# Kernel tuning notes

Measured on AMD Instinct MI355X. Metric: run time of the kernel, lower is better.

Reference implementation:

```python
import jax, jax.numpy as jnp
import numpy as np

NUM_HEADS = 16

def setup_inputs() -> dict:
    key = jax.random.key(0)
    ks = jax.random.split(key, 6)
    B, S, D = 2, 2048, 1024
    scale = 1.0 / np.sqrt(D)
    x = jax.random.normal(ks[0], (B, S, D), dtype=jnp.float32)
    mask = jnp.tril(jnp.ones((S, S), dtype=jnp.int32))[None, None, :, :]  # causal [1,1,S,S]
    Wq = jax.random.normal(ks[1], (D, D), dtype=jnp.float32) * scale
    Wk = jax.random.normal(ks[2], (D, D), dtype=jnp.float32) * scale
    Wv = jax.random.normal(ks[3], (D, D), dtype=jnp.float32) * scale
    Wo = jax.random.normal(ks[4], (D, D), dtype=jnp.float32) * scale
    z = jnp.zeros((D,), dtype=jnp.float32)
    return {"x": x, "mask": mask, "Wq": Wq, "bq": z, "Wk": Wk, "bk": z,
            "Wv": Wv, "bv": z, "Wo": Wo, "bo": z}

def reference(x, mask, Wq, bq, Wk, bk, Wv, bv, Wo, bo):
    B, S, D = x.shape
    H = NUM_HEADS
    hd = D // H
    # torch Linear: y = x @ W.T + b
    def proj(W, b):
        return (x @ W.T + b).reshape(B, S, H, hd).transpose(0, 2, 1, 3)  # [B,H,S,hd]
    q = proj(Wq, bq)
    k = proj(Wk, bk)
    v = proj(Wv, bv)
    # NOTE: original module does NOT scale by 1/sqrt(d_k) -- faithful to source.
    scores = jnp.einsum('bhqd,bhkd->bhqk', q, k)  # [B,H,S,S]
    scores = jnp.where(mask == 0, jnp.float32(-10000.0), scores)
    attn = jax.nn.softmax(scores, axis=-1)
    # dropout omitted for deterministic reference (eval-mode equivalent)
    out = jnp.einsum('bhqk,bhkd->bhqd', attn, v)
    out = out.transpose(0, 2, 1, 3).reshape(B, S, D)
    return out @ Wo.T + bo
```

## Files before the change

### kernel.cpp

```cpp
#include <hip/hip_runtime.h>

#define S_LEN 2048
#define DM    1024
#define NHEAD 16
#define HDIM  64
#define NB    2
#define NROWS (NB * S_LEN)
#define RCP_LN2 1.44269504f

using f32x4  = __attribute__((ext_vector_type(4))) float;
using f16x8  = __attribute__((ext_vector_type(8))) _Float16;

__device__ __forceinline__ ushort f2h(float f) {
  return __builtin_bit_cast(ushort, (_Float16)f);
}
__device__ __forceinline__ unsigned pkrtz(float a, float b) {
  return __builtin_bit_cast(unsigned, __builtin_amdgcn_cvt_pkrtz(a, b));
}
__device__ __forceinline__ float fexp2(float x) {
  return __builtin_amdgcn_exp2f(x);
}
__device__ __forceinline__ f32x4 mfma16(f16x8 a, f16x8 b, f32x4 c) {
  return __builtin_amdgcn_mfma_f32_16x16x32_f16(a, b, c, 0, 0, 0);
}
__device__ __forceinline__ void async16(const ushort* g, ushort* l) {
  __builtin_amdgcn_global_load_lds(
      (const __attribute__((address_space(1))) unsigned*)g,
      (__attribute__((address_space(3))) unsigned*)l, 16, 0, 0);
}

__device__ const int g_qi_tab[24] = {15,15,7,14,14,13,13,6,12,12,11,11,
                                     5,10,10,9,9,4,8,8,3,2,1,0};
__device__ const int g_hf_tab[24] = {0,1,2,0,1,0,1,2,0,1,0,1,
                                     2,0,1,0,1,2,0,1,2,2,2,2};

__global__ void tohalf5(const float* __restrict__ x,  const float* __restrict__ wq,
                        const float* __restrict__ wk, const float* __restrict__ wv,
                        const float* __restrict__ wo,
                        ushort* __restrict__ Xh, ushort* __restrict__ Wh,
                        ushort* __restrict__ Woh) {
  constexpr int X4 = (NROWS * DM) / 4;
  constexpr int W4 = (DM * DM) / 4;
  const size_t WN = (size_t)DM * DM;
  int i = blockIdx.x * 256 + threadIdx.x;
  const float4* src; ushort4* dst; int k;
  if (i < X4)               { src = (const float4*)x;  dst = (ushort4*)Xh;        k = i; }
  else if (i < X4 + W4)     { src = (const float4*)wq; dst = (ushort4*)Wh;        k = i - X4; }
  else if (i < X4 + 2*W4)   { src = (const float4*)wk; dst = (ushort4*)(Wh+WN);   k = i - X4 - W4; }
  else if (i < X4 + 3*W4)   { src = (const float4*)wv; dst = (ushort4*)(Wh+2*WN); k = i - X4 - 2*W4; }
  else                      { src = (const float4*)wo; dst = (ushort4*)Woh;       k = i - X4 - 3*W4; }
  float4 v = src[k];
  dst[k] = make_ushort4(f2h(v.x), f2h(v.y), f2h(v.z), f2h(v.w));
}

template<int EPI, int MFRAG, int NFRAG>
__global__ __launch_bounds__(256, 2)
void gemm_half(const ushort* __restrict__ A, const ushort* __restrict__ B,
               const float* __restrict__ biasQ, const float* __restrict__ biasK,
               const float* __restrict__ biasV,
               float* __restrict__ outF,
               ushort* __restrict__ Q, ushort* __restrict__ Kd,
               ushort* __restrict__ Vt, int Ncols)
{
  constexpr int KD = 1024;
  constexpr int BM = MFRAG * 32, BN = NFRAG * 32;
  constexpr int NCH = (BM + BN) / 8;
  constexpr int CPW = NCH / 4;
  __shared__ ushort sL[(BM + BN) * 64];
  const int t = threadIdx.x;
  const int w = t >> 6, l = t & 63;
  const int lr = l >> 4, lc = l & 15;
  const int wr = w >> 1, wc = w & 1;
  const int nwg = gridDim.x * gridDim.y;
  const int lin = blockIdx.y * gridDim.x + blockIdx.x;
  const int per8 = nwg >> 3;
  const int swz = (lin & 7) * per8 + (lin >> 3);
  const int i0 = (swz / gridDim.x) * BM, j0 = (swz % gridDim.x) * BN;

  const int srow = l >> 3;
  const int se   = ((l & 7) ^ srow) << 3;

  const ushort* sp[CPW];
#pragma unroll
  for (int ii = 0; ii < CPW; ++ii) {
    const int c = w * CPW + ii;
    sp[ii] = (c < BM / 8)
        ? A + (size_t)(i0 + c * 8 + srow) * KD + se
        : B + (size_t)(j0 + (c - BM / 8) * 8 + srow) * KD + se;
  }

  f32x4 acc[MFRAG][NFRAG] = {};

  for (int k0 = 0; k0 < KD; k0 += 64) {
#pragma unroll
    for (int ii = 0; ii < CPW; ++ii) {
      async16(sp[ii], &sL[(w * CPW + ii) * 512]);
      sp[ii] += 64;
    }
    asm volatile("s_waitcnt vmcnt(0)" ::: "memory");
    __syncthreads();
#pragma unroll
    for (int kk = 0; kk < 2; ++kk) {
      const int cb = (kk * 64 + lr * 16) ^ ((lc & 7) << 4);
      f16x8 a[MFRAG], b[NFRAG];
#pragma unroll
      for (int m = 0; m < MFRAG; ++m)
        a[m] = *(const f16x8*)&sL[(wr * MFRAG * 16 + m * 16 + lc) * 64 + (cb >> 1)];
#pragma unroll
      for (int n = 0; n < NFRAG; ++n)
        b[n] = *(const f16x8*)&sL[BM * 64 + (wc * NFRAG * 16 + n * 16 + lc) * 64 + (cb >> 1)];
      __builtin_amdgcn_s_setprio(1);
#pragma unroll
      for (int m = 0; m < MFRAG; ++m)
#pragma unroll
        for (int n = 0; n < NFRAG; ++n)
          acc[m][n] = mfma16(a[m], b[n], acc[m][n]);
      __builtin_amdgcn_s_setprio(0);
    }
    __syncthreads();
  }

#pragma unroll
  for (int m = 0; m < MFRAG; ++m)
#pragma unroll
    for (int n = 0; n < NFRAG; ++n) {
      const int jbase = j0 + wc * NFRAG * 16 + n * 16;
      const int ibase = i0 + wr * MFRAG * 16 + m * 16 + lr * 4;
      if constexpr (EPI == 0) {
        const int region = jbase >> 10;
        const int jc0 = jbase & 1023;
        const int h = jc0 >> 6, d0 = jc0 & 63;
        const int b = ibase >> 11, s0 = ibase & 2047;
        const size_t bh = (size_t)(b * NHEAD + h);
        if (region == 0) {
          float bb = biasQ[jc0 + lc];
#pragma unroll
          for (int r = 0; r < 4; ++r)
            Q[(bh * S_LEN + s0 + r) * HDIM + d0 + lc] =
                f2h((acc[m][n][r] + bb) * RCP_LN2);
        } else if (region == 1) {
          float bb = biasK[jc0 + lc];
#pragma unroll
          for (int r = 0; r < 4; ++r)
            Kd[(bh * S_LEN + s0 + r) * HDIM + d0 + lc] = f2h(acc[m][n][r] + bb);
        } else {
          float bb = biasV[jc0 + lc];
          ushort4 pv = make_ushort4(f2h(acc[m][n][0] + bb), f2h(acc[m][n][1] + bb),
                                    f2h(acc[m][n][2] + bb), f2h(acc[m][n][3] + bb));
          *(ushort4*)&Vt[(bh * HDIM + d0 + lc) * S_LEN + s0] = pv;
        }
      } else {
#pragma unroll
        for (int r = 0; r < 4; ++r)
          outF[(size_t)(ibase + r) * Ncols + jbase + lc] =
              acc[m][n][r] + biasQ[jbase + lc];
      }
    }
}

__global__ __launch_bounds__(256, 3)
void attn_kernel(const ushort* __restrict__ Qp, const ushort* __restrict__ Kp,
                 const ushort* __restrict__ Vt, ushort* __restrict__ O,
                 float* __restrict__ Pacc, float* __restrict__ Pml)
{
  __shared__ ushort sKV[2][2 * 64 * 64];
  __shared__ ushort Plds[4][2][16][72];
  const int blk = blockIdx.x;
  const int c = blk & 255, s3 = blk >> 8;
  const int rank = (s3 == 0) ? c : ((s3 == 1) ? 511 - c : 512 + c);
  const int ty = rank >> 5, bh = rank & 31;
  const int qi = g_qi_tab[ty], hf = g_hf_tab[ty];
  const int nkt = 2 * qi + 2;
  const int kt0 = (hf == 1) ? (nkt >> 1) : 0;
  const int kt1 = (hf == 0) ? (nkt >> 1) : nkt;

  const int t = threadIdx.x, w = t >> 6, l = t & 63;
  const int g = l >> 4, q = l & 15;
  const size_t base = (size_t)bh * S_LEN * HDIM;
  const int q0w = qi * 128 + w * 32;

  const int srow = l >> 3;
  const int se   = ((l & 7) ^ srow) << 3;

  const int sel = w >> 1;
  const ushort* sp[4];
  const int sadv = (sel == 0) ? 64 * HDIM : 64;
#pragma unroll
  for (int ii = 0; ii < 4; ++ii) {
    const int sub = (w * 4 + ii) & 7;
    sp[ii] = (sel == 0)
        ? Kp + base + (size_t)(kt0 * 64 + sub * 8 + srow) * HDIM + se
        : Vt + ((size_t)bh * HDIM + sub * 8 + srow) * S_LEN + kt0 * 64 + se;
  }

  auto stage = [&](int buf) {
#pragma unroll
    for (int ii = 0; ii < 4; ++ii) {
      const int sub = (w * 4 + ii) & 7;
      async16(sp[ii], &sKV[buf][sel * 4096 + sub * 512]);
      sp[ii] += sadv;
    }
  };

  f16x8 bQ[2][2];
#pragma unroll
  for (int u = 0; u < 2; ++u)
#pragma unroll
    for (int ks = 0; ks < 2; ++ks)
      bQ[u][ks] = *(const f16x8*)(Qp + base +
                  (size_t)(q0w + u * 16 + q) * HDIM + ks * 32 + g * 8);

  f32x4 oacc[2][4] = {};
  float m[2] = {-3e38f, -3e38f}, lsum[2] = {0.f, 0.f};

  stage(0);
  asm volatile("s_waitcnt vmcnt(0)" ::: "memory");
  __syncthreads();
  int cur = 0;

  for (int kt = kt0; kt < kt1; ++kt) {
    if (kt + 1 < kt1) stage(cur ^ 1);

    if (kt * 64 <= q0w + 31) {
      f32x4 s[2][4] = {};
      __builtin_amdgcn_s_setprio(1);
#pragma unroll
      for (int ks = 0; ks < 2; ++ks) {
        const int cb = (((ks * 64 + g * 16) ^ ((q & 7) << 4)) >> 1);
#pragma unroll
        for (int n = 0; n < 4; ++n) {
          f16x8 kf = *(const f16x8*)&sKV[cur][(n * 16 + q) * 64 + cb];
          s[0][n] = mfma16(kf, bQ[0][ks], s[0][n]);
          s[1][n] = mfma16(kf, bQ[1][ks], s[1][n]);
        }
      }
      __builtin_amdgcn_s_setprio(0);
#pragma unroll
      for (int u = 0; u < 2; ++u) {
        if (kt * 64 + 63 > q0w + u * 16) {
          const int qg = q0w + u * 16 + q;
#pragma unroll
          for (int n = 0; n < 4; ++n)
#pragma unroll
            for (int r = 0; r < 4; ++r) {
              int kg = kt * 64 + n * 16 + g * 4 + r;
              if (kg > qg) s[u][n][r] = -1e30f;
            }
        }
      }
      float pm[2];
#pragma unroll
      for (int u = 0; u < 2; ++u) {
        float p = -3e38f;
#pragma unroll
        for (int n = 0; n < 4; ++n)
          p = fmaxf(p, fmaxf(fmaxf(s[u][n][0], s[u][n][1]),
                             fmaxf(s[u][n][2], s[u][n][3])));
        pm[u] = p;
      }
#pragma unroll
      for (int u = 0; u < 2; ++u) {
        if (__any(pm[u] > m[u] + 8.0f)) {
          float pf = pm[u];
          pf = fmaxf(pf, __shfl_xor(pf, 16));
          pf = fmaxf(pf, __shfl_xor(pf, 32));
          float mnew = fmaxf(m[u], pf);
          float sc = fexp2(m[u] - mnew);
          m[u] = mnew;
          float scr[4];
#pragma unroll
          for (int r = 0; r < 4; ++r) scr[r] = __shfl(sc, g * 4 + r);
#pragma unroll
          for (int dt = 0; dt < 4; ++dt)
#pragma unroll
            for (int r = 0; r < 4; ++r) oacc[u][dt][r] *= scr[r];
          lsum[u] *= sc;
        }
      }
#pragma unroll
      for (int u = 0; u < 2; ++u) {
        float rs = 0.f;
#pragma unroll
        for (int n = 0; n < 4; ++n)
#pragma unroll
          for (int r = 0; r < 4; ++r) {
            float pe = fexp2(s[u][n][r] - m[u]);
            s[u][n][r] = pe;
            rs += pe;
          }
        lsum[u] += rs;
      }
#pragma unroll
      for (int u = 0; u < 2; ++u)
#pragma unroll
        for (int n = 0; n < 4; ++n) {
          uint2 pk = make_uint2(pkrtz(s[u][n][0], s[u][n][1]),
                                pkrtz(s[u][n][2], s[u][n][3]));
          *(uint2*)&Plds[w][u][q][n * 16 + g * 4] = pk;
        }
      __builtin_amdgcn_s_setprio(1);
#pragma unroll
      for (int ks = 0; ks < 2; ++ks) {
        const int cb = (((ks * 64 + g * 16) ^ ((q & 7) << 4)) >> 1);
        f16x8 ap0 = *(const f16x8*)&Plds[w][0][q][ks * 32 + g * 8];
        f16x8 ap1 = *(const f16x8*)&Plds[w][1][q][ks * 32 + g * 8];
#pragma unroll
        for (int dt = 0; dt < 4; ++dt) {
          f16x8 bv = *(const f16x8*)&sKV[cur][4096 + (dt * 16 + q) * 64 + cb];
          oacc[0][dt] = mfma16(ap0, bv, oacc[0][dt]);
          oacc[1][dt] = mfma16(ap1, bv, oacc[1][dt]);
        }
      }
      __builtin_amdgcn_s_setprio(0);
    }
    asm volatile("s_waitcnt vmcnt(0)" ::: "memory");
    __syncthreads();
    cur ^= 1;
  }

#pragma unroll
  for (int u = 0; u < 2; ++u) {
    lsum[u] += __shfl_xor(lsum[u], 16);
    lsum[u] += __shfl_xor(lsum[u], 32);
  }

  if (hf == 2) {
    const int b = bh >> 4, h = bh & 15;
#pragma unroll
    for (int u = 0; u < 2; ++u) {
      float lsr[4];
#pragma unroll
      for (int r = 0; r < 4; ++r)
        lsr[r] = __builtin_amdgcn_rcpf(__shfl(lsum[u], g * 4 + r));
#pragma unroll
      for (int dt = 0; dt < 4; ++dt)
#pragma unroll
        for (int r = 0; r < 4; ++r) {
          int qg = q0w + u * 16 + g * 4 + r;
          O[((size_t)b * S_LEN + qg) * DM + h * HDIM + dt * 16 + q] =
              f2h(oacc[u][dt][r] * lsr[r]);
        }
    }
  } else {
    const int pidx = (bh * 8 + (qi - 8)) * 2 + hf;
    float* po = Pacc + (size_t)pidx * (128 * 64);
#pragma unroll
    for (int u = 0; u < 2; ++u) {
#pragma unroll
      for (int dt = 0; dt < 4; ++dt)
#pragma unroll
        for (int r = 0; r < 4; ++r)
          po[(w * 32 + u * 16 + g * 4 + r) * 64 + dt * 16 + q] = oacc[u][dt][r];
      if (g == 0) {
        Pml[(size_t)pidx * 256 + (w * 32 + u * 16 + q) * 2]     = m[u];
        Pml[(size_t)pidx * 256 + (w * 32 + u * 16 + q) * 2 + 1] = lsum[u];
      }
    }
  }
}

__global__ void combine_kernel(const float* __restrict__ Pacc,
                               const float* __restrict__ Pml,
                               ushort* __restrict__ O)
{
  int gid = blockIdx.x * 256 + threadIdx.x;
  int row = gid >> 6, col = gid & 63;
  int bh = row >> 10;
  int rr = row & 1023;
  int qi = 8 + (rr >> 7), qr = rr & 127;
  int p0 = (bh * 8 + (qi - 8)) * 2;
  float m1 = Pml[(size_t)p0 * 256 + qr * 2];
  float l1 = Pml[(size_t)p0 * 256 + qr * 2 + 1];
  float m2 = Pml[(size_t)(p0 + 1) * 256 + qr * 2];
  float l2 = Pml[(size_t)(p0 + 1) * 256 + qr * 2 + 1];
  float o1 = Pacc[(size_t)p0 * 8192 + qr * 64 + col];
  float o2 = Pacc[(size_t)(p0 + 1) * 8192 + qr * 64 + col];
  float mf = fmaxf(m1, m2);
  float e1 = fexp2(m1 - mf), e2 = fexp2(m2 - mf);
  float o = o1 * e1 + o2 * e2;
  float lden = l1 * e1 + l2 * e2;
  int b = bh >> 4, h = bh & 15;
  O[((size_t)b * S_LEN + qi * 128 + qr) * DM + h * HDIM + col] = f2h(o / lden);
}

extern "C" void kernel_launch(void* const* d_in, const int* in_sizes, int n_in,
                              void* d_out, int out_size, void* d_ws, size_t ws_size,
                              hipStream_t stream)
{
  const float* x  = (const float*)d_in[0];
  const float* Wq = (const float*)d_in[2];
  const float* bq = (const float*)d_in[3];
  const float* Wk = (const float*)d_in[4];
  const float* bk = (const float*)d_in[5];
  const float* Wv = (const float*)d_in[6];
  const float* bv = (const float*)d_in[7];
  const float* Wo = (const float*)d_in[8];
  const float* bo = (const float*)d_in[9];
  float* out = (float*)d_out;

  char* ws = (char*)d_ws;
  size_t off = 0;
  auto alloc = [&](size_t bytes) { char* p = ws + off; off += bytes; return p; };
  const size_t XN = (size_t)NROWS * DM;
  const size_t WN = (size_t)DM * DM;

  ushort* Xh  = (ushort*)alloc(XN * 2);
  ushort* Wh  = (ushort*)alloc(3 * WN * 2);
  ushort* Woh = (ushort*)alloc(WN * 2);
  ushort* Qb  = (ushort*)alloc(XN * 2);
  ushort* Kb  = (ushort*)alloc(XN * 2);
  ushort* Vt  = (ushort*)alloc(XN * 2);
  ushort* Ob  = (ushort*)alloc(XN * 2);
  float*  Pacc = (float*)alloc((size_t)512 * 128 * 64 * 4);
  float*  Pml  = (float*)alloc((size_t)512 * 256 * 4);
  (void)ws_size; (void)in_sizes; (void)n_in; (void)out_size;

  const int total4 = (int)(XN / 4 + 4 * (WN / 4));
  tohalf5<<<total4 / 256, 256, 0, stream>>>(x, Wq, Wk, Wv, Wo, Xh, Wh, Woh);

  gemm_half<0, 4, 4><<<dim3(24, 32), 256, 0, stream>>>(
      Xh, Wh, bq, bk, bv, nullptr, Qb, Kb, Vt, 3072);
  attn_kernel<<<768, 256, 0, stream>>>(Qb, Kb, Vt, Ob, Pacc, Pml);
  combine_kernel<<<8192, 256, 0, stream>>>(Pacc, Pml, Ob);
  gemm_half<1, 2, 2><<<dim3(16, 64), 256, 0, stream>>>(
      Ob, Woh, bo, nullptr, nullptr, out, nullptr, nullptr, nullptr, 1024);
}
```

Baseline: 101.8 us.

## Rebalance causal attention into 38 KV-split work units with universal combine

```diff
diff --git a/kernel.cpp b/kernel.cpp
--- a/kernel.cpp
+++ b/kernel.cpp
@@ -7,12 +7,16 @@
 #define NB    2
 #define NROWS (NB * S_LEN)
 #define RCP_LN2 1.44269504f
+#define NTY   38
 
 using f32x4  = __attribute__((ext_vector_type(4))) float;
 using f16x8  = __attribute__((ext_vector_type(8))) _Float16;
 
 __device__ __forceinline__ ushort f2h(float f) {
   return __builtin_bit_cast(ushort, (_Float16)f);
+}
+__device__ __forceinline__ float h2f(ushort u) {
+  return (float)__builtin_bit_cast(_Float16, u);
 }
 __device__ __forceinline__ unsigned pkrtz(float a, float b) {
   return __builtin_bit_cast(unsigned, __builtin_amdgcn_cvt_pkrtz(a, b));
@@ -29,10 +33,21 @@
       (__attribute__((address_space(3))) unsigned*)l, 16, 0, 0);
 }
 
-__device__ const int g_qi_tab[24] = {15,15,7,14,14,13,13,6,12,12,11,11,
-                                     5,10,10,9,9,4,8,8,3,2,1,0};
-__device__ const int g_hf_tab[24] = {0,1,2,0,1,0,1,2,0,1,0,1,
-                                     2,0,1,0,1,2,0,1,2,2,2,2};
+__device__ const int g_qi[NTY] = {
+  8,8,12,12, 15,15,15,15,14,14,12,11,11,11,10,7,7,3,
+  14,14,13,13,13,13,10,10,9,9,6,6, 9,5,5,2, 4,4, 1, 0};
+__device__ const int g_k0[NTY] = {
+  0,9,0,9, 0,8,16,24,0,15,18,0,8,16,0,0,8,0,
+  8,23,0,7,14,21,8,15,0,7,0,7, 14,0,6,0, 0,5, 0, 0};
+__device__ const int g_k1[NTY] = {
+  9,18,9,18, 8,16,24,32,8,23,26,8,16,24,8,8,16,8,
+  15,30,7,14,21,28,15,22,7,14,7,14, 20,6,12,6, 5,10, 4, 2};
+__device__ const int g_cnt[16] = {1,1,1,1,2,2,2,2,2,3,3,3,3,4,4,4};
+__device__ const int g_cmb[16][4] = {
+  {37,37,37,37},{36,36,36,36},{33,33,33,33},{17,17,17,17},
+  {34,35,35,35},{31,32,32,32},{28,29,29,29},{15,16,16,16},{0,1,1,1},
+  {26,27,30,30},{14,24,25,25},{11,12,13,13},{2,3,10,10},
+  {20,21,22,23},{8,18,9,19},{4,5,6,7}};
 
 __global__ void tohalf5(const float* __restrict__ x,  const float* __restrict__ wq,
                         const float* __restrict__ wk, const float* __restrict__ wv,
@@ -158,26 +173,23 @@
     }
 }
 
-__global__ __launch_bounds__(256, 3)
+__global__ __launch_bounds__(256, 4)
 void attn_kernel(const ushort* __restrict__ Qp, const ushort* __restrict__ Kp,
-                 const ushort* __restrict__ Vt, ushort* __restrict__ O,
-                 float* __restrict__ Pacc, float* __restrict__ Pml)
+                 const ushort* __restrict__ Vt,
+                 ushort* __restrict__ Pacc, float* __restrict__ Pml)
 {
   __shared__ ushort sKV[2][2 * 64 * 64];
-  __shared__ ushort Plds[4][2][16][72];
+  __shared__ ushort Plds[4][16][64];
   const int blk = blockIdx.x;
-  const int c = blk & 255, s3 = blk >> 8;
-  const int rank = (s3 == 0) ? c : ((s3 == 1) ? 511 - c : 512 + c);
-  const int ty = rank >> 5, bh = rank & 31;
-  const int qi = g_qi_tab[ty], hf = g_hf_tab[ty];
-  const int nkt = 2 * qi + 2;
-  const int kt0 = (hf == 1) ? (nkt >> 1) : 0;
-  const int kt1 = (hf == 0) ? (nkt >> 1) : nkt;
+  const int ty = blk >> 5, bh = blk & 31;
+  const int qi = g_qi[ty];
+  const int kt0 = g_k0[ty], kt1 = g_k1[ty];
 
   const int t = threadIdx.x, w = t >> 6, l = t & 63;
   const int g = l >> 4, q = l & 15;
   const size_t base = (size_t)bh * S_LEN * HDIM;
   const int q0w = qi * 128 + w * 32;
+  const int psw = (q & 7) << 3;
 
   const int srow = l >> 3;
   const int se   = ((l & 7) ^ srow) << 3;
@@ -291,27 +303,26 @@
         lsum[u] += rs;
       }
 #pragma unroll
-      for (int u = 0; u < 2; ++u)
+      for (int u = 0; u < 2; ++u) {
 #pragma unroll
         for (int n = 0; n < 4; ++n) {
           uint2 pk = make_uint2(pkrtz(s[u][n][0], s[u][n][1]),
                                 pkrtz(s[u][n][2], s[u][n][3]));
-          *(uint2*)&Plds[w][u][q][n * 16 + g * 4] = pk;
-        }
-      __builtin_amdgcn_s_setprio(1);
-#pragma unroll
-      for (int ks = 0; ks < 2; ++ks) {
-        const int cb = (((ks * 64 + g * 16) ^ ((q & 7) << 4)) >> 1);
-        f16x8 ap0 = *(const f16x8*)&Plds[w][0][q][ks * 32 + g * 8];
-        f16x8 ap1 = *(const f16x8*)&Plds[w][1][q][ks * 32 + g * 8];
-#pragma unroll
-        for (int dt = 0; dt < 4; ++dt) {
-          f16x8 bv = *(const f16x8*)&sKV[cur][4096 + (dt * 16 + q) * 64 + cb];
-          oacc[0][dt] = mfma16(ap0, bv, oacc[0][dt]);
-          oacc[1][dt] = mfma16(ap1, bv, oacc[1][dt]);
-        }
-      }
-      __builtin_amdgcn_s_setprio(0);
+          *(uint2*)&Plds[w][q][(n * 16 + g * 4) ^ psw] = pk;
+        }
+        __builtin_amdgcn_s_setprio(1);
+#pragma unroll
+        for (int ks = 0; ks < 2; ++ks) {
+          f16x8 ap = *(const f16x8*)&Plds[w][q][(ks * 32 + g * 8) ^ psw];
+          const int cb = (((ks * 64 + g * 16) ^ ((q & 7) << 4)) >> 1);
+#pragma unroll
+          for (int dt = 0; dt < 4; ++dt) {
+            f16x8 bv = *(const f16x8*)&sKV[cur][4096 + (dt * 16 + q) * 64 + cb];
+            oacc[u][dt] = mfma16(ap, bv, oacc[u][dt]);
+          }
+        }
+        __builtin_amdgcn_s_setprio(0);
+      }
     }
     asm volatile("s_waitcnt vmcnt(0)" ::: "memory");
     __syncthreads();
@@ -323,64 +334,53 @@
     lsum[u] += __shfl_xor(lsum[u], 16);
     lsum[u] += __shfl_xor(lsum[u], 32);
   }
-
-  if (hf == 2) {
-    const int b = bh >> 4, h = bh & 15;
-#pragma unroll
-    for (int u = 0; u < 2; ++u) {
-      float lsr[4];
+  const int pidx = bh * NTY + ty;
+  ushort* po = Pacc + (size_t)pidx * (128 * 64);
+#pragma unroll
+  for (int u = 0; u < 2; ++u) {
+#pragma unroll
+    for (int dt = 0; dt < 4; ++dt)
 #pragma unroll
       for (int r = 0; r < 4; ++r)
-        lsr[r] = __builtin_amdgcn_rcpf(__shfl(lsum[u], g * 4 + r));
-#pragma unroll
-      for (int dt = 0; dt < 4; ++dt)
-#pragma unroll
-        for (int r = 0; r < 4; ++r) {
-          int qg = q0w + u * 16 + g * 4 + r;
-          O[((size_t)b * S_LEN + qg) * DM + h * HDIM + dt * 16 + q] =
-              f2h(oacc[u][dt][r] * lsr[r]);
-        }
-    }
-  } else {
-    const int pidx = (bh * 8 + (qi - 8)) * 2 + hf;
-    float* po = Pacc + (size_t)pidx * (128 * 64);
-#pragma unroll
-    for (int u = 0; u < 2; ++u) {
-#pragma unroll
-      for (int dt = 0; dt < 4; ++dt)
-#pragma unroll
-        for (int r = 0; r < 4; ++r)
-          po[(w * 32 + u * 16 + g * 4 + r) * 64 + dt * 16 + q] = oacc[u][dt][r];
-      if (g == 0) {
-        Pml[(size_t)pidx * 256 + (w * 32 + u * 16 + q) * 2]     = m[u];
-        Pml[(size_t)pidx * 256 + (w * 32 + u * 16 + q) * 2 + 1] = lsum[u];
-      }
-    }
-  }
-}
-
-__global__ void combine_kernel(const float* __restrict__ Pacc,
+        po[(w * 32 + u * 16 + g * 4 + r) * 64 + dt * 16 + q] = f2h(oacc[u][dt][r]);
+    if (g == 0) {
+      Pml[(size_t)pidx * 256 + (w * 32 + u * 16 + q) * 2]     = m[u];
+      Pml[(size_t)pidx * 256 + (w * 32 + u * 16 + q) * 2 + 1] = lsum[u];
+    }
+  }
+}
+
+__global__ void combine_kernel(const ushort* __restrict__ Pacc,
                                const float* __restrict__ Pml,
                                ushort* __restrict__ O)
 {
   int gid = blockIdx.x * 256 + threadIdx.x;
-  int row = gid >> 6, col = gid & 63;
-  int bh = row >> 10;
-  int rr = row & 1023;
-  int qi = 8 + (rr >> 7), qr = rr & 127;
-  int p0 = (bh * 8 + (qi - 8)) * 2;
-  float m1 = Pml[(size_t)p0 * 256 + qr * 2];
-  float l1 = Pml[(size_t)p0 * 256 + qr * 2 + 1];
-  float m2 = Pml[(size_t)(p0 + 1) * 256 + qr * 2];
-  float l2 = Pml[(size_t)(p0 + 1) * 256 + qr * 2 + 1];
-  float o1 = Pacc[(size_t)p0 * 8192 + qr * 64 + col];
-  float o2 = Pacc[(size_t)(p0 + 1) * 8192 + qr * 64 + col];
-  float mf = fmaxf(m1, m2);
-  float e1 = fexp2(m1 - mf), e2 = fexp2(m2 - mf);
-  float o = o1 * e1 + o2 * e2;
-  float lden = l1 * e1 + l2 * e2;
+  int col = gid & 63;
+  int row = (gid >> 6) & 2047;
+  int bh  = gid >> 17;
+  int qi = row >> 7, qr = row & 127;
+  int cnt = g_cnt[qi];
+  float mv[4], lv[4], ov[4];
+  float mf = -3e38f;
+#pragma unroll
+  for (int p = 0; p < 4; ++p) {
+    if (p < cnt) {
+      int pidx = bh * NTY + g_cmb[qi][p];
+      mv[p] = Pml[(size_t)pidx * 256 + qr * 2];
+      lv[p] = Pml[(size_t)pidx * 256 + qr * 2 + 1];
+      ov[p] = h2f(Pacc[(size_t)pidx * 8192 + qr * 64 + col]);
+      mf = fmaxf(mf, mv[p]);
+    } else { mv[p] = -3e38f; lv[p] = 0.f; ov[p] = 0.f; }
+  }
+  float osum = 0.f, lden = 0.f;
+#pragma unroll
+  for (int p = 0; p < 4; ++p) {
+    float e = fexp2(mv[p] - mf);
+    osum += ov[p] * e;
+    lden += lv[p] * e;
+  }
   int b = bh >> 4, h = bh & 15;
-  O[((size_t)b * S_LEN + qi * 128 + qr) * DM + h * HDIM + col] = f2h(o / lden);
+  O[((size_t)b * S_LEN + row) * DM + h * HDIM + col] = f2h(osum / lden);
 }
 
 extern "C" void kernel_launch(void* const* d_in, const int* in_sizes, int n_in,
@@ -411,8 +411,8 @@
   ushort* Kb  = (ushort*)alloc(XN * 2);
   ushort* Vt  = (ushort*)alloc(XN * 2);
   ushort* Ob  = (ushort*)alloc(XN * 2);
-  float*  Pacc = (float*)alloc((size_t)512 * 128 * 64 * 4);
-  float*  Pml  = (float*)alloc((size_t)512 * 256 * 4);
+  ushort* Pacc = (ushort*)alloc((size_t)32 * NTY * 128 * 64 * 2);
+  float*  Pml  = (float*)alloc((size_t)32 * NTY * 256 * 4);
   (void)ws_size; (void)in_sizes; (void)n_in; (void)out_size;
 
   const int total4 = (int)(XN / 4 + 4 * (WN / 4));
@@ -420,8 +420,8 @@
 
   gemm_half<0, 4, 4><<<dim3(24, 32), 256, 0, stream>>>(
       Xh, Wh, bq, bk, bv, nullptr, Qb, Kb, Vt, 3072);
-  attn_kernel<<<768, 256, 0, stream>>>(Qb, Kb, Vt, Ob, Pacc, Pml);
-  combine_kernel<<<8192, 256, 0, stream>>>(Pacc, Pml, Ob);
+  attn_kernel<<<NTY * 32, 256, 0, stream>>>(Qb, Kb, Vt, Pacc, Pml);
+  combine_kernel<<<16384, 256, 0, stream>>>(Pacc, Pml, Ob);
   gemm_half<1, 2, 2><<<dim3(16, 64), 256, 0, stream>>>(
       Ob, Woh, bo, nullptr, nullptr, out, nullptr, nullptr, nullptr, 1024);
 }
```

Measured after the change: 119.2 us. 1.17x slower.

## Load K/V fragments directly from global memory instead of LDS double buffering

Applied to the files above, without the earlier changes.

```diff
diff --git a/kernel.cpp b/kernel.cpp
--- a/kernel.cpp
+++ b/kernel.cpp
@@ -158,12 +158,11 @@
     }
 }
 
-__global__ __launch_bounds__(256, 3)
+__global__ __launch_bounds__(256, 4)
 void attn_kernel(const ushort* __restrict__ Qp, const ushort* __restrict__ Kp,
                  const ushort* __restrict__ Vt, ushort* __restrict__ O,
                  float* __restrict__ Pacc, float* __restrict__ Pml)
 {
-  __shared__ ushort sKV[2][2 * 64 * 64];
   __shared__ ushort Plds[4][2][16][72];
   const int blk = blockIdx.x;
   const int c = blk & 255, s3 = blk >> 8;
@@ -179,28 +178,8 @@
   const size_t base = (size_t)bh * S_LEN * HDIM;
   const int q0w = qi * 128 + w * 32;
 
-  const int srow = l >> 3;
-  const int se   = ((l & 7) ^ srow) << 3;
-
-  const int sel = w >> 1;
-  const ushort* sp[4];
-  const int sadv = (sel == 0) ? 64 * HDIM : 64;
-#pragma unroll
-  for (int ii = 0; ii < 4; ++ii) {
-    const int sub = (w * 4 + ii) & 7;
-    sp[ii] = (sel == 0)
-        ? Kp + base + (size_t)(kt0 * 64 + sub * 8 + srow) * HDIM + se
-        : Vt + ((size_t)bh * HDIM + sub * 8 + srow) * S_LEN + kt0 * 64 + se;
-  }
-
-  auto stage = [&](int buf) {
-#pragma unroll
-    for (int ii = 0; ii < 4; ++ii) {
-      const int sub = (w * 4 + ii) & 7;
-      async16(sp[ii], &sKV[buf][sel * 4096 + sub * 512]);
-      sp[ii] += sadv;
-    }
-  };
+  const ushort* kp = Kp + base + (size_t)(kt0 * 64 + q) * HDIM + g * 8;
+  const ushort* vp = Vt + ((size_t)bh * HDIM + q) * S_LEN + (size_t)kt0 * 64 + g * 8;
 
   f16x8 bQ[2][2];
 #pragma unroll
@@ -213,23 +192,15 @@
   f32x4 oacc[2][4] = {};
   float m[2] = {-3e38f, -3e38f}, lsum[2] = {0.f, 0.f};
 
-  stage(0);
-  asm volatile("s_waitcnt vmcnt(0)" ::: "memory");
-  __syncthreads();
-  int cur = 0;
-
   for (int kt = kt0; kt < kt1; ++kt) {
-    if (kt + 1 < kt1) stage(cur ^ 1);
-
     if (kt * 64 <= q0w + 31) {
       f32x4 s[2][4] = {};
       __builtin_amdgcn_s_setprio(1);
 #pragma unroll
       for (int ks = 0; ks < 2; ++ks) {
-        const int cb = (((ks * 64 + g * 16) ^ ((q & 7) << 4)) >> 1);
 #pragma unroll
         for (int n = 0; n < 4; ++n) {
-          f16x8 kf = *(const f16x8*)&sKV[cur][(n * 16 + q) * 64 + cb];
+          f16x8 kf = *(const f16x8*)(kp + n * 16 * HDIM + ks * 32);
           s[0][n] = mfma16(kf, bQ[0][ks], s[0][n]);
           s[1][n] = mfma16(kf, bQ[1][ks], s[1][n]);
         }
@@ -301,21 +272,19 @@
       __builtin_amdgcn_s_setprio(1);
 #pragma unroll
       for (int ks = 0; ks < 2; ++ks) {
-        const int cb = (((ks * 64 + g * 16) ^ ((q & 7) << 4)) >> 1);
         f16x8 ap0 = *(const f16x8*)&Plds[w][0][q][ks * 32 + g * 8];
         f16x8 ap1 = *(const f16x8*)&Plds[w][1][q][ks * 32 + g * 8];
 #pragma unroll
         for (int dt = 0; dt < 4; ++dt) {
-          f16x8 bv = *(const f16x8*)&sKV[cur][4096 + (dt * 16 + q) * 64 + cb];
+          f16x8 bv = *(const f16x8*)(vp + (size_t)dt * 16 * S_LEN + ks * 32);
           oacc[0][dt] = mfma16(ap0, bv, oacc[0][dt]);
           oacc[1][dt] = mfma16(ap1, bv, oacc[1][dt]);
         }
       }
       __builtin_amdgcn_s_setprio(0);
     }
-    asm volatile("s_waitcnt vmcnt(0)" ::: "memory");
-    __syncthreads();
-    cur ^= 1;
+    kp += 64 * HDIM;
+    vp += 64;
   }
 
 #pragma unroll
```

After: 136.5 us. +34.1%, slower.
